# Kernel tuning notes

Hardware: AMD Instinct MI355X
Metric: run time of the kernel (lower is better)

## Reference

```python
import jax, jax.numpy as jnp
import numpy as np

N_NODES = 50000


def _gcn_norm(edge_index, num_nodes):
    # Add self-loops (PyG GCNConv default) and compute symmetric norm.
    loops = jnp.arange(num_nodes, dtype=edge_index.dtype)
    src = jnp.concatenate([edge_index[0], loops])
    dst = jnp.concatenate([edge_index[1], loops])
    ones = jnp.ones(src.shape[0], dtype=jnp.float32)
    deg = jax.ops.segment_sum(ones, dst, num_segments=num_nodes)
    deg_inv_sqrt = jnp.where(deg > 0, jax.lax.rsqrt(jnp.maximum(deg, 1.0)), 0.0)
    norm = deg_inv_sqrt[src] * deg_inv_sqrt[dst]  # [E + N]
    return src, dst, norm


def _gcn_conv(x, src, dst, norm, W, b, num_nodes):
    xw = x @ W                               # [N, out]
    msg = xw[src] * norm[:, None]            # gather + scale  [E+N, out]
    out = jax.ops.segment_sum(msg, dst, num_segments=num_nodes)  # scatter-add
    return out + b


def setup_inputs() -> dict:
    key = jax.random.key(0)
    ks = jax.random.split(key, 10)
    d_in, d_h, d_out = 64, 64, 8
    n_edges = 800000
    x = jax.random.normal(ks[0], (N_NODES, d_in), dtype=jnp.float32)
    edge_index = jax.random.randint(ks[1], (2, n_edges), 0, N_NODES, dtype=jnp.int64)
    def w(k, fan_in, fan_out):
        return jax.random.normal(k, (fan_in, fan_out), dtype=jnp.float32) * (1.0 / np.sqrt(fan_in))
    return {
        "x": x,
        "edge_index": edge_index,
        "W0": w(ks[2], d_in, d_h), "b0": jnp.zeros((d_h,), jnp.float32),
        "W1": w(ks[3], d_h, d_h), "b1": jnp.zeros((d_h,), jnp.float32),
        "W2": w(ks[4], d_h, d_h), "b2": jnp.zeros((d_h,), jnp.float32),
        "linW": w(ks[5], d_h, d_out), "linb": jnp.zeros((d_out,), jnp.float32),
    }


def reference(x, edge_index, W0, b0, W1, b1, W2, b2, linW, linb):
    num_nodes = x.shape[0]
    src, dst, norm = _gcn_norm(edge_index, num_nodes)
    # 3 GCNConv layers, ReLU; dropout is identity at inference (training=False).
    for W, b in ((W0, b0), (W1, b1), (W2, b2)):
        x = jax.nn.relu(_gcn_conv(x, src, dst, norm, W, b, num_nodes))
    return x @ linW + linb
```

## Files before the change

kernel.cpp:

```cpp
#include <hip/hip_runtime.h>
#include <hip/hip_fp16.h>

#define TPB 256
#define CAP 16384
#define CAPSH 14


__device__ __forceinline__ int ld_idx(const void* p, long long i, int is64) {
    return is64 ? (int)((const long long*)p)[i] : ((const int*)p)[i];
}

__device__ __forceinline__ float4 h4_to_f4(ushort4 v) {
    float4 r;
    r.x = __half2float(__ushort_as_half(v.x));
    r.y = __half2float(__ushort_as_half(v.y));
    r.z = __half2float(__ushort_as_half(v.z));
    r.w = __half2float(__ushort_as_half(v.w));
    return r;
}

__device__ __forceinline__ ushort4 f4_to_h4(float4 v) {
    ushort4 r;
    r.x = __half_as_ushort(__float2half_rn(v.x));
    r.y = __half_as_ushort(__float2half_rn(v.y));
    r.z = __half_as_ushort(__float2half_rn(v.z));
    r.w = __half_as_ushort(__float2half_rn(v.w));
    return r;
}

__global__ __launch_bounds__(TPB) void p3_scatter(const void* ei, long long E,
                                                  int* gcur, int* pairs) {
    __shared__ int cnt[TPB];
    __shared__ int cur2[TPB];
    __shared__ int s_is64;
    int t = threadIdx.x;
    if (t < 64) {
        const unsigned int* w = (const unsigned int*)ei;
        unsigned long long m = __ballot(w[2 * t + 1] != 0u);
        if (t == 0) s_is64 = (m == 0ull) ? 1 : 0;
    }
    cnt[t] = 0;
    __syncthreads();
    const int is64 = s_is64;
    long long chunk = (E + gridDim.x - 1) / gridDim.x;
    long long s0 = (long long)blockIdx.x * chunk;
    long long s1 = (s0 + chunk < E) ? s0 + chunk : E;
    for (long long e = s0 + t; e < s1; e += TPB) {
        int d = ld_idx(ei, E + e, is64);
        atomicAdd(&cnt[d >> 8], 1);
    }
    __syncthreads();
    if (cnt[t]) cur2[t] = (t << CAPSH) + atomicAdd(&gcur[t], cnt[t]);
    __syncthreads();
    for (long long e = s0 + t; e < s1; e += TPB) {
        int sv = ld_idx(ei, e, is64);
        int d  = ld_idx(ei, E + e, is64);
        int pos = atomicAdd(&cur2[d >> 8], 1);
        pairs[pos] = (sv << 8) | (d & 255);
    }
}

__global__ __launch_bounds__(TPB) void p4_fill(const int* __restrict__ pairs,
                                               const int* __restrict__ gcur,
                                               const float* __restrict__ x,
                                               int2* __restrict__ meta,
                                               int* __restrict__ csr,
                                               ushort4* __restrict__ z0, int N) {
    __shared__ int ldeg[TPB];
    __shared__ int ssc[TPB];
    __shared__ int cur[TPB];
    __shared__ float fdis[TPB];
    int t = threadIdx.x;
    int b = blockIdx.x;
    int base = b << CAPSH;
    int ecnt = gcur[b];
    ldeg[t] = 0;
    __syncthreads();
    for (int e = base + t; e < base + ecnt; e += TPB)
        atomicAdd(&ldeg[pairs[e] & 255], 1);
    __syncthreads();
    int dv = ldeg[t];
    int pv = (dv + 15) & ~15;
    ssc[t] = pv;
    __syncthreads();
    for (int off = 1; off < TPB; off <<= 1) {
        int u = 0;
        if (t >= off) u = ssc[t - off];
        __syncthreads();
        ssc[t] += u;
        __syncthreads();
    }
    int o = base + ssc[t] - pv;
    cur[t] = o;
    float dd = rsqrtf((float)(dv + 1));
    fdis[t] = dd;
    int node = (b << 8) + t;
    if (node < N)
        meta[node] = make_int2((o << 7) | (pv >> 4), __float_as_int(dd));
    __syncthreads();
    for (int e = base + t; e < base + ecnt; e += TPB) {
        int p = pairs[e];
        int pos = atomicAdd(&cur[p & 255], 1);
        csr[pos] = p >> 8;
    }
    for (int e = o + dv; e < o + pv; ++e) csr[e] = N;

    int ni = t >> 4, c = t & 15;
    for (int p = 0; p < 16; ++p) {
        int nd = (b << 8) + p * 16 + ni;
        if (nd < N) {
            float dvv = fdis[p * 16 + ni];
            float4 h = ((const float4*)x)[nd * 16 + c];
            float4 r = {h.x * dvv, h.y * dvv, h.z * dvv, h.w * dvv};
            z0[nd * 16 + c] = f4_to_h4(r);
        }
    }
    if (b == 0 && t < 16) z0[(size_t)N * 16 + t] = make_ushort4(0, 0, 0, 0);
}

__device__ __forceinline__ float4 gather_rows(const ushort4* __restrict__ y4,
                                              const int* __restrict__ csr,
                                              int start, int nbatch, int c,
                                              float4 acc) {
    const int base = threadIdx.x & 48;
    for (int bt = 0; bt < nbatch; ++bt) {
        int idx = csr[start + bt * 16 + c];
        #pragma unroll
        for (int k = 0; k < 16; ++k) {
            int s = __shfl(idx, base + k);
            float4 v = h4_to_f4(y4[s * 16 + c]);
            acc.x += v.x; acc.y += v.y; acc.z += v.z; acc.w += v.w;
        }
    }
    return acc;
}

__device__ __forceinline__ float4 shfl_mm(float4 s, const float4* Ws4, int c) {
    const int base = threadIdx.x & 48;
    float4 u = {0.f, 0.f, 0.f, 0.f};
    #pragma unroll
    for (int r = 0; r < 4; ++r) {
        float sr = (r == 0) ? s.x : (r == 1) ? s.y : (r == 2) ? s.z : s.w;
        #pragma unroll
        for (int q = 0; q < 16; ++q) {
            float hv = __shfl(sr, base + q);
            float4 w = Ws4[(q * 4 + r) * 16 + c];
            u.x = fmaf(hv, w.x, u.x);
            u.y = fmaf(hv, w.y, u.y);
            u.z = fmaf(hv, w.z, u.z);
            u.w = fmaf(hv, w.w, u.w);
        }
    }
    return u;
}

__global__ __launch_bounds__(TPB) void layer_mm(const ushort4* __restrict__ z,
                                                const int* __restrict__ csr,
                                                const int2* __restrict__ meta,
                                                const float* __restrict__ b,
                                                const float* __restrict__ W,
                                                ushort4* __restrict__ zout, int n) {
    __shared__ float Ws[64 * 64];
    int t = threadIdx.x;
    float4* Ws4 = (float4*)Ws;
    const float4* W4g = (const float4*)W;
    #pragma unroll
    for (int i = 0; i < 4; ++i) Ws4[t + i * TPB] = W4g[t + i * TPB];

    if (blockIdx.x == 0 && t < 16)
        zout[(size_t)n * 16 + t] = make_ushort4(0, 0, 0, 0);

    int ni = t >> 4, c = t & 15;
    int node = blockIdx.x * 16 + ni;
    float4 s = {0.f, 0.f, 0.f, 0.f};
    float dv = 0.f;
    if (node < n) {
        int2 m = meta[node];
        int start = ((unsigned)m.x) >> 7;
        int nbatch = m.x & 127;
        dv = __int_as_float(m.y);
        s = h4_to_f4(z[node * 16 + c]);
        s = gather_rows(z, csr, start, nbatch, c, s);
    }
    __syncthreads();
    float4 u = shfl_mm(s, Ws4, c);
    if (node < n) {
        float4 bb = ((const float4*)b)[c];
        float4 r;
        r.x = fmaxf(fmaf(dv, u.x, bb.x), 0.f) * dv;
        r.y = fmaxf(fmaf(dv, u.y, bb.y), 0.f) * dv;
        r.z = fmaxf(fmaf(dv, u.z, bb.z), 0.f) * dv;
        r.w = fmaxf(fmaf(dv, u.w, bb.w), 0.f) * dv;
        zout[node * 16 + c] = f4_to_h4(r);
    }
}

__global__ __launch_bounds__(TPB) void layer_final(const ushort4* __restrict__ z,
                                                   const int* __restrict__ csr,
                                                   const int2* __restrict__ meta,
                                                   const float* __restrict__ b,
                                                   const float* __restrict__ W,
                                                   const float* __restrict__ Wl,
                                                   const float* __restrict__ bl,
                                                   float* __restrict__ out, int n) {
    __shared__ float Ws[64 * 64];
    __shared__ float Wls[64 * 8];
    __shared__ float bls[8];
    int t = threadIdx.x;
    float4* Ws4 = (float4*)Ws;
    const float4* W4g = (const float4*)W;
    #pragma unroll
    for (int i = 0; i < 4; ++i) Ws4[t + i * TPB] = W4g[t + i * TPB];
    if (t < 128) ((float4*)Wls)[t] = ((const float4*)Wl)[t];
    if (t < 8) bls[t] = bl[t];

    int ni = t >> 4, c = t & 15;
    int node = blockIdx.x * 16 + ni;
    float4 s = {0.f, 0.f, 0.f, 0.f};
    float dv = 0.f;
    if (node < n) {
        int2 m = meta[node];
        int start = ((unsigned)m.x) >> 7;
        int nbatch = m.x & 127;
        dv = __int_as_float(m.y);
        s = h4_to_f4(z[node * 16 + c]);
        s = gather_rows(z, csr, start, nbatch, c, s);
    }
    __syncthreads();
    float4 u = shfl_mm(s, Ws4, c);
    float4 bb = ((const float4*)b)[c];
    float4 h;
    h.x = fmaxf(fmaf(dv, u.x, bb.x), 0.f);
    h.y = fmaxf(fmaf(dv, u.y, bb.y), 0.f);
    h.z = fmaxf(fmaf(dv, u.z, bb.z), 0.f);
    h.w = fmaxf(fmaf(dv, u.w, bb.w), 0.f);

    const int base = threadIdx.x & 48;
    int col = c & 7;
    float acc = bls[col];
    #pragma unroll
    for (int r = 0; r < 4; ++r) {
        float hr = (r == 0) ? h.x : (r == 1) ? h.y : (r == 2) ? h.z : h.w;
        #pragma unroll
        for (int q = 0; q < 16; ++q) {
            float hv = __shfl(hr, base + q);
            acc = fmaf(hv, Wls[(q * 4 + r) * 8 + col], acc);
        }
    }
    if (c < 8 && node < n) out[node * 8 + col] = acc;
}

extern "C" void kernel_launch(void* const* d_in, const int* in_sizes, int n_in,
                              void* d_out, int out_size, void* d_ws, size_t ws_size,
                              hipStream_t stream) {
    const float* x  = (const float*)d_in[0];
    const void*  ei = d_in[1];
    const float* W0 = (const float*)d_in[2];
    const float* b0 = (const float*)d_in[3];
    const float* W1 = (const float*)d_in[4];
    const float* b1 = (const float*)d_in[5];
    const float* W2 = (const float*)d_in[6];
    const float* b2 = (const float*)d_in[7];
    const float* Wl = (const float*)d_in[8];
    const float* bl = (const float*)d_in[9];

    const long long E = in_sizes[1] / 2;
    const int dh = in_sizes[3];
    const int din = in_sizes[2] / dh;
    const int N = in_sizes[0] / din;
    const int nb = (N + 255) >> 8;

    char* ws = (char*)d_ws;
    size_t off = 0;
    auto alloc = [&](size_t bytes) -> char* {
        char* r = ws + off;
        off += (bytes + 255) & ~(size_t)255;
        return r;
    };
    int*     gcur    = (int*)    alloc(1024);
    int2*    meta    = (int2*)   alloc((size_t)N * 8);
    int*     pairs   = (int*)    alloc((size_t)nb * CAP * 4);
    int*     csr     = (int*)    alloc((size_t)nb * CAP * 4);
    ushort4* zbA     = (ushort4*)alloc((size_t)(N + 1) * 64 * 2);
    ushort4* zbB     = (ushort4*)alloc((size_t)(N + 1) * 64 * 2);

    hipMemsetAsync(gcur, 0, 256 * sizeof(int), stream);
    p3_scatter<<<256, TPB, 0, stream>>>(ei, E, gcur, pairs);
    p4_fill<<<nb, TPB, 0, stream>>>(pairs, gcur, x, meta, csr, zbA, N);

    const int gL = (N + 15) / 16;
    layer_mm<<<gL, TPB, 0, stream>>>(zbA, csr, meta, b0, W0, zbB, N);
    layer_mm<<<gL, TPB, 0, stream>>>(zbB, csr, meta, b1, W1, zbA, N);
    layer_final<<<gL, TPB, 0, stream>>>(zbA, csr, meta, b2, W2, Wl, bl,
                                        (float*)d_out, N);
}
```

Baseline: 212.3 us.

## Split feature columns into halves so each gather pass fits in cache

Measured after the change: 251.9 us. 18.6% more time.

```diff
diff --git a/kernel.cpp b/kernel.cpp
--- a/kernel.cpp
+++ b/kernel.cpp
@@ -5,18 +5,12 @@
 #define CAP 16384
 #define CAPSH 14
 
+typedef float    f32x4  __attribute__((ext_vector_type(4)));
+typedef unsigned short u16x4 __attribute__((ext_vector_type(4)));
+
 
 __device__ __forceinline__ int ld_idx(const void* p, long long i, int is64) {
     return is64 ? (int)((const long long*)p)[i] : ((const int*)p)[i];
-}
-
-__device__ __forceinline__ float4 h4_to_f4(ushort4 v) {
-    float4 r;
-    r.x = __half2float(__ushort_as_half(v.x));
-    r.y = __half2float(__ushort_as_half(v.y));
-    r.z = __half2float(__ushort_as_half(v.z));
-    r.w = __half2float(__ushort_as_half(v.w));
-    return r;
 }
 
 __device__ __forceinline__ ushort4 f4_to_h4(float4 v) {
@@ -28,6 +22,14 @@
     return r;
 }
 
+__device__ __forceinline__ void nt_store_h4(ushort4* p, ushort4 v) {
+    __builtin_nontemporal_store(*(u16x4*)&v, (u16x4*)p);
+}
+
+__device__ __forceinline__ void nt_store_f4(float4* p, float4 v) {
+    __builtin_nontemporal_store(*(f32x4*)&v, (f32x4*)p);
+}
+
 __global__ __launch_bounds__(TPB) void p3_scatter(const void* ei, long long E,
                                                   int* gcur, int* pairs) {
     __shared__ int cnt[TPB];
@@ -65,7 +67,8 @@
                                                const float* __restrict__ x,
                                                int2* __restrict__ meta,
                                                int* __restrict__ csr,
-                                               ushort4* __restrict__ z0, int N) {
+                                               ushort4* __restrict__ zlo,
+                                               ushort4* __restrict__ zhi, int N) {
     __shared__ int ldeg[TPB];
     __shared__ int ssc[TPB];
     __shared__ int cur[TPB];
@@ -110,132 +113,194 @@
         int nd = (b << 8) + p * 16 + ni;
         if (nd < N) {
             float dvv = fdis[p * 16 + ni];
-            float4 h = ((const float4*)x)[nd * 16 + c];
+            float4 h = ((const float4*)x)[(size_t)nd * 16 + c];
             float4 r = {h.x * dvv, h.y * dvv, h.z * dvv, h.w * dvv};
-            z0[nd * 16 + c] = f4_to_h4(r);
+            ushort4 hv = f4_to_h4(r);
+            if (c < 8) nt_store_h4(&zlo[(size_t)nd * 8 + c], hv);
+            else       nt_store_h4(&zhi[(size_t)nd * 8 + (c - 8)], hv);
         }
     }
-    if (b == 0 && t < 16) z0[(size_t)N * 16 + t] = make_ushort4(0, 0, 0, 0);
-}
-
-__device__ __forceinline__ float4 gather_rows(const ushort4* __restrict__ y4,
+    if (b == 0 && t < 8)  nt_store_h4(&zlo[(size_t)N * 8 + t], make_ushort4(0,0,0,0));
+    if (b == 0 && t >= 8 && t < 16)
+        nt_store_h4(&zhi[(size_t)N * 8 + (t - 8)], make_ushort4(0,0,0,0));
+}
+
+__device__ __forceinline__ float2 gather_half(const ushort2* __restrict__ z,
                                               const int* __restrict__ csr,
                                               int start, int nbatch, int c,
-                                              float4 acc) {
+                                              float2 s) {
     const int base = threadIdx.x & 48;
     for (int bt = 0; bt < nbatch; ++bt) {
-        int idx = csr[start + bt * 16 + c];
+        int idx = __builtin_nontemporal_load(csr + start + bt * 16 + c);
         #pragma unroll
         for (int k = 0; k < 16; ++k) {
-            int s = __shfl(idx, base + k);
-            float4 v = h4_to_f4(y4[s * 16 + c]);
-            acc.x += v.x; acc.y += v.y; acc.z += v.z; acc.w += v.w;
+            int si = __shfl(idx, base + k);
+            ushort2 v = z[(size_t)si * 16 + c];
+            s.x += __half2float(__ushort_as_half(v.x));
+            s.y += __half2float(__ushort_as_half(v.y));
         }
     }
-    return acc;
-}
-
-__device__ __forceinline__ float4 shfl_mm(float4 s, const float4* Ws4, int c) {
-    const int base = threadIdx.x & 48;
-    float4 u = {0.f, 0.f, 0.f, 0.f};
-    #pragma unroll
-    for (int r = 0; r < 4; ++r) {
-        float sr = (r == 0) ? s.x : (r == 1) ? s.y : (r == 2) ? s.z : s.w;
-        #pragma unroll
-        for (int q = 0; q < 16; ++q) {
-            float hv = __shfl(sr, base + q);
-            float4 w = Ws4[(q * 4 + r) * 16 + c];
-            u.x = fmaf(hv, w.x, u.x);
-            u.y = fmaf(hv, w.y, u.y);
-            u.z = fmaf(hv, w.z, u.z);
-            u.w = fmaf(hv, w.w, u.w);
-        }
-    }
-    return u;
-}
-
-__global__ __launch_bounds__(TPB) void layer_mm(const ushort4* __restrict__ z,
+    return s;
+}
+
+__global__ __launch_bounds__(TPB) void layer_lo(const ushort2* __restrict__ zlo,
                                                 const int* __restrict__ csr,
                                                 const int2* __restrict__ meta,
-                                                const float* __restrict__ b,
                                                 const float* __restrict__ W,
-                                                ushort4* __restrict__ zout, int n) {
-    __shared__ float Ws[64 * 64];
+                                                float4* __restrict__ u, int n) {
+    __shared__ float Ws[32 * 64];
     int t = threadIdx.x;
     float4* Ws4 = (float4*)Ws;
     const float4* W4g = (const float4*)W;
-    #pragma unroll
-    for (int i = 0; i < 4; ++i) Ws4[t + i * TPB] = W4g[t + i * TPB];
-
-    if (blockIdx.x == 0 && t < 16)
-        zout[(size_t)n * 16 + t] = make_ushort4(0, 0, 0, 0);
+    Ws4[t] = W4g[t];
+    Ws4[t + 256] = W4g[t + 256];
 
     int ni = t >> 4, c = t & 15;
     int node = blockIdx.x * 16 + ni;
-    float4 s = {0.f, 0.f, 0.f, 0.f};
+    float2 s = {0.f, 0.f};
+    if (node < n) {
+        int2 m = meta[node];
+        int start = ((unsigned)m.x) >> 7;
+        int nbatch = m.x & 127;
+        ushort2 v = zlo[(size_t)node * 16 + c];
+        s.x = __half2float(__ushort_as_half(v.x));
+        s.y = __half2float(__ushort_as_half(v.y));
+        s = gather_half(zlo, csr, start, nbatch, c, s);
+    }
+    __syncthreads();
+    const int base = t & 48;
+    float4 ua = {0.f, 0.f, 0.f, 0.f};
+    #pragma unroll
+    for (int q = 0; q < 16; ++q) {
+        float a = __shfl(s.x, base + q);
+        float b = __shfl(s.y, base + q);
+        float4 w0 = Ws4[(2 * q) * 16 + c];
+        float4 w1 = Ws4[(2 * q + 1) * 16 + c];
+        ua.x = fmaf(a, w0.x, fmaf(b, w1.x, ua.x));
+        ua.y = fmaf(a, w0.y, fmaf(b, w1.y, ua.y));
+        ua.z = fmaf(a, w0.z, fmaf(b, w1.z, ua.z));
+        ua.w = fmaf(a, w0.w, fmaf(b, w1.w, ua.w));
+    }
+    if (node < n) nt_store_f4(&u[(size_t)node * 16 + c], ua);
+}
+
+__global__ __launch_bounds__(TPB) void layer_hi(const ushort2* __restrict__ zhi,
+                                                const int* __restrict__ csr,
+                                                const int2* __restrict__ meta,
+                                                const float* __restrict__ W,
+                                                const float* __restrict__ b,
+                                                const float4* __restrict__ u,
+                                                ushort4* __restrict__ zolo,
+                                                ushort4* __restrict__ zohi, int n) {
+    __shared__ float Ws[32 * 64];
+    int t = threadIdx.x;
+    float4* Ws4 = (float4*)Ws;
+    const float4* W4g = (const float4*)W;
+    Ws4[t] = W4g[512 + t];
+    Ws4[t + 256] = W4g[768 + t];
+
+    if (blockIdx.x == 0 && t < 8)
+        nt_store_h4(&zolo[(size_t)n * 8 + t], make_ushort4(0,0,0,0));
+    if (blockIdx.x == 0 && t >= 8 && t < 16)
+        nt_store_h4(&zohi[(size_t)n * 8 + (t - 8)], make_ushort4(0,0,0,0));
+
+    int ni = t >> 4, c = t & 15;
+    int node = blockIdx.x * 16 + ni;
+    float2 s = {0.f, 0.f};
     float dv = 0.f;
     if (node < n) {
         int2 m = meta[node];
         int start = ((unsigned)m.x) >> 7;
         int nbatch = m.x & 127;
         dv = __int_as_float(m.y);
-        s = h4_to_f4(z[node * 16 + c]);
-        s = gather_rows(z, csr, start, nbatch, c, s);
-    }
-    __syncthreads();
-    float4 u = shfl_mm(s, Ws4, c);
+        ushort2 v = zhi[(size_t)node * 16 + c];
+        s.x = __half2float(__ushort_as_half(v.x));
+        s.y = __half2float(__ushort_as_half(v.y));
+        s = gather_half(zhi, csr, start, nbatch, c, s);
+    }
+    __syncthreads();
+    const int base = t & 48;
+    float4 ua = {0.f, 0.f, 0.f, 0.f};
+    #pragma unroll
+    for (int q = 0; q < 16; ++q) {
+        float a = __shfl(s.x, base + q);
+        float bqv = __shfl(s.y, base + q);
+        float4 w0 = Ws4[(2 * q) * 16 + c];
+        float4 w1 = Ws4[(2 * q + 1) * 16 + c];
+        ua.x = fmaf(a, w0.x, fmaf(bqv, w1.x, ua.x));
+        ua.y = fmaf(a, w0.y, fmaf(bqv, w1.y, ua.y));
+        ua.z = fmaf(a, w0.z, fmaf(bqv, w1.z, ua.z));
+        ua.w = fmaf(a, w0.w, fmaf(bqv, w1.w, ua.w));
+    }
     if (node < n) {
+        f32x4 up = __builtin_nontemporal_load((const f32x4*)&u[(size_t)node * 16 + c]);
         float4 bb = ((const float4*)b)[c];
         float4 r;
-        r.x = fmaxf(fmaf(dv, u.x, bb.x), 0.f) * dv;
-        r.y = fmaxf(fmaf(dv, u.y, bb.y), 0.f) * dv;
-        r.z = fmaxf(fmaf(dv, u.z, bb.z), 0.f) * dv;
-        r.w = fmaxf(fmaf(dv, u.w, bb.w), 0.f) * dv;
-        zout[node * 16 + c] = f4_to_h4(r);
-    }
-}
-
-__global__ __launch_bounds__(TPB) void layer_final(const ushort4* __restrict__ z,
-                                                   const int* __restrict__ csr,
-                                                   const int2* __restrict__ meta,
-                                                   const float* __restrict__ b,
-                                                   const float* __restrict__ W,
-                                                   const float* __restrict__ Wl,
-                                                   const float* __restrict__ bl,
-                                                   float* __restrict__ out, int n) {
-    __shared__ float Ws[64 * 64];
+        r.x = fmaxf(fmaf(dv, ua.x + up.x, bb.x), 0.f) * dv;
+        r.y = fmaxf(fmaf(dv, ua.y + up.y, bb.y), 0.f) * dv;
+        r.z = fmaxf(fmaf(dv, ua.z + up.z, bb.z), 0.f) * dv;
+        r.w = fmaxf(fmaf(dv, ua.w + up.w, bb.w), 0.f) * dv;
+        ushort4 hv = f4_to_h4(r);
+        if (c < 8) nt_store_h4(&zolo[(size_t)node * 8 + c], hv);
+        else       nt_store_h4(&zohi[(size_t)node * 8 + (c - 8)], hv);
+    }
+}
+
+__global__ __launch_bounds__(TPB) void layer_hi_final(
+        const ushort2* __restrict__ zhi, const int* __restrict__ csr,
+        const int2* __restrict__ meta, const float* __restrict__ W,
+        const float* __restrict__ b, const float4* __restrict__ u,
+        const float* __restrict__ Wl, const float* __restrict__ bl,
+        float* __restrict__ out, int n) {
+    __shared__ float Ws[32 * 64];
     __shared__ float Wls[64 * 8];
     __shared__ float bls[8];
     int t = threadIdx.x;
     float4* Ws4 = (float4*)Ws;
     const float4* W4g = (const float4*)W;
-    #pragma unroll
-    for (int i = 0; i < 4; ++i) Ws4[t + i * TPB] = W4g[t + i * TPB];
+    Ws4[t] = W4g[512 + t];
+    Ws4[t + 256] = W4g[768 + t];
     if (t < 128) ((float4*)Wls)[t] = ((const float4*)Wl)[t];
     if (t < 8) bls[t] = bl[t];
 
     int ni = t >> 4, c = t & 15;
     int node = blockIdx.x * 16 + ni;
-    float4 s = {0.f, 0.f, 0.f, 0.f};
+    float2 s = {0.f, 0.f};
     float dv = 0.f;
     if (node < n) {
         int2 m = meta[node];
         int start = ((unsigned)m.x) >> 7;
         int nbatch = m.x & 127;
         dv = __int_as_float(m.y);
-        s = h4_to_f4(z[node * 16 + c]);
-        s = gather_rows(z, csr, start, nbatch, c, s);
-    }
-    __syncthreads();
-    float4 u = shfl_mm(s, Ws4, c);
+        ushort2 v = zhi[(size_t)node * 16 + c];
+        s.x = __half2float(__ushort_as_half(v.x));
+        s.y = __half2float(__ushort_as_half(v.y));
+        s = gather_half(zhi, csr, start, nbatch, c, s);
+    }
+    __syncthreads();
+    const int base = t & 48;
+    float4 ua = {0.f, 0.f, 0.f, 0.f};
+    #pragma unroll
+    for (int q = 0; q < 16; ++q) {
+        float a = __shfl(s.x, base + q);
+        float bqv = __shfl(s.y, base + q);
+        float4 w0 = Ws4[(2 * q) * 16 + c];
+        float4 w1 = Ws4[(2 * q + 1) * 16 + c];
+        ua.x = fmaf(a, w0.x, fmaf(bqv, w1.x, ua.x));
+        ua.y = fmaf(a, w0.y, fmaf(bqv, w1.y, ua.y));
+        ua.z = fmaf(a, w0.z, fmaf(bqv, w1.z, ua.z));
+        ua.w = fmaf(a, w0.w, fmaf(bqv, w1.w, ua.w));
+    }
+    f32x4 up = {0.f, 0.f, 0.f, 0.f};
+    if (node < n)
+        up = __builtin_nontemporal_load((const f32x4*)&u[(size_t)node * 16 + c]);
     float4 bb = ((const float4*)b)[c];
     float4 h;
-    h.x = fmaxf(fmaf(dv, u.x, bb.x), 0.f);
-    h.y = fmaxf(fmaf(dv, u.y, bb.y), 0.f);
-    h.z = fmaxf(fmaf(dv, u.z, bb.z), 0.f);
-    h.w = fmaxf(fmaf(dv, u.w, bb.w), 0.f);
-
-    const int base = threadIdx.x & 48;
+    h.x = fmaxf(fmaf(dv, ua.x + up.x, bb.x), 0.f);
+    h.y = fmaxf(fmaf(dv, ua.y + up.y, bb.y), 0.f);
+    h.z = fmaxf(fmaf(dv, ua.z + up.z, bb.z), 0.f);
+    h.w = fmaxf(fmaf(dv, ua.w + up.w, bb.w), 0.f);
+
     int col = c & 7;
     float acc = bls[col];
     #pragma unroll
@@ -247,7 +312,7 @@
             acc = fmaf(hv, Wls[(q * 4 + r) * 8 + col], acc);
         }
     }
-    if (c < 8 && node < n) out[node * 8 + col] = acc;
+    if (c < 8 && node < n) out[(size_t)node * 8 + col] = acc;
 }
 
 extern "C" void kernel_launch(void* const* d_in, const int* in_sizes, int n_in,
@@ -277,20 +342,28 @@
         off += (bytes + 255) & ~(size_t)255;
         return r;
     };
-    int*     gcur    = (int*)    alloc(1024);
-    int2*    meta    = (int2*)   alloc((size_t)N * 8);
-    int*     pairs   = (int*)    alloc((size_t)nb * CAP * 4);
-    int*     csr     = (int*)    alloc((size_t)nb * CAP * 4);
-    ushort4* zbA     = (ushort4*)alloc((size_t)(N + 1) * 64 * 2);
-    ushort4* zbB     = (ushort4*)alloc((size_t)(N + 1) * 64 * 2);
+    int*     gcur  = (int*)    alloc(1024);
+    int2*    meta  = (int2*)   alloc((size_t)N * 8);
+    int*     pairs = (int*)    alloc((size_t)nb * CAP * 4);
+    int*     csr   = (int*)    alloc((size_t)nb * CAP * 4);
+    ushort4* zAlo  = (ushort4*)alloc((size_t)(N + 1) * 64);
+    ushort4* zAhi  = (ushort4*)alloc((size_t)(N + 1) * 64);
+    ushort4* zBlo  = (ushort4*)alloc((size_t)(N + 1) * 64);
+    ushort4* zBhi  = (ushort4*)alloc((size_t)(N + 1) * 64);
+    float4*  u     = (float4*) alloc((size_t)N * 256);
 
     hipMemsetAsync(gcur, 0, 256 * sizeof(int), stream);
     p3_scatter<<<256, TPB, 0, stream>>>(ei, E, gcur, pairs);
-    p4_fill<<<nb, TPB, 0, stream>>>(pairs, gcur, x, meta, csr, zbA, N);
+    p4_fill<<<nb, TPB, 0, stream>>>(pairs, gcur, x, meta, csr, zAlo, zAhi, N);
 
     const int gL = (N + 15) / 16;
-    layer_mm<<<gL, TPB, 0, stream>>>(zbA, csr, meta, b0, W0, zbB, N);
-    layer_mm<<<gL, TPB, 0, stream>>>(zbB, csr, meta, b1, W1, zbA, N);
-    layer_final<<<gL, TPB, 0, stream>>>(zbA, csr, meta, b2, W2, Wl, bl,
-                                        (float*)d_out, N);
-}
+    layer_lo<<<gL, TPB, 0, stream>>>((const ushort2*)zAlo, csr, meta, W0, u, N);
+    layer_hi<<<gL, TPB, 0, stream>>>((const ushort2*)zAhi, csr, meta, W0, b0, u,
+                                     zBlo, zBhi, N);
+    layer_lo<<<gL, TPB, 0, stream>>>((const ushort2*)zBlo, csr, meta, W1, u, N);
+    layer_hi<<<gL, TPB, 0, stream>>>((const ushort2*)zBhi, csr, meta, W1, b1, u,
+                                     zAlo, zAhi, N);
+    layer_lo<<<gL, TPB, 0, stream>>>((const ushort2*)zAlo, csr, meta, W2, u, N);
+    layer_hi_final<<<gL, TPB, 0, stream>>>((const ushort2*)zAhi, csr, meta, W2,
+                                           b2, u, Wl, bl, (float*)d_out, N);
+}
```
